# Kernel tuning notes

Measured on AMD Instinct MI355X. Metric: run time of the kernel, lower is better.

## Reference

```python
import jax, jax.numpy as jnp
import numpy as np

NL, D, NH, HD, MLP, L = 4, 1280, 16, 80, 5120, 2048
SEG = 512  # patches per packed image


def setup_inputs() -> dict:
    key = jax.random.key(0)
    ks = jax.random.split(key, 16)
    s = 0.02
    # per-segment RoPE frequency table: positions restart at each image boundary
    inv_freq = 1.0 / (10000.0 ** (jnp.arange(0, HD, 2, dtype=jnp.float32) / HD))  # (HD/2,)
    pos = (jnp.arange(L) % SEG).astype(jnp.float32)
    rotary_pos_emb = pos[:, None] * inv_freq[None, :]  # (L, HD/2)
    return {
        "x": jax.random.normal(ks[0], (L, D), jnp.float32),
        "rotary_pos_emb": rotary_pos_emb,
        "cu_seqlens": jnp.array([0, 512, 1024, 1536, 2048], jnp.int32),
        "ln1_g": 1.0 + s * jax.random.normal(ks[1], (NL, D), jnp.float32),
        "ln1_b": s * jax.random.normal(ks[2], (NL, D), jnp.float32),
        "ln2_g": 1.0 + s * jax.random.normal(ks[3], (NL, D), jnp.float32),
        "ln2_b": s * jax.random.normal(ks[4], (NL, D), jnp.float32),
        "qkv_w": s * jax.random.normal(ks[5], (NL, 3 * D, D), jnp.float32),
        "qkv_b": s * jax.random.normal(ks[6], (NL, 3 * D), jnp.float32),
        "proj_w": s * jax.random.normal(ks[7], (NL, D, D), jnp.float32),
        "proj_b": s * jax.random.normal(ks[8], (NL, D), jnp.float32),
        "mlp_w1": s * jax.random.normal(ks[9], (NL, MLP, D), jnp.float32),
        "mlp_b1": s * jax.random.normal(ks[10], (NL, MLP), jnp.float32),
        "mlp_w2": s * jax.random.normal(ks[11], (NL, D, MLP), jnp.float32),
        "mlp_b2": s * jax.random.normal(ks[12], (NL, D), jnp.float32),
    }


def _ln(x, g, b):
    m = jnp.mean(x, axis=-1, keepdims=True)
    v = jnp.mean((x - m) ** 2, axis=-1, keepdims=True)
    return (x - m) * jax.lax.rsqrt(v + 1e-6) * g + b


def _rope(t, cos, sin):
    # t: (L, H, HD); cos/sin: (L, 1, HD)
    half = t.shape[-1] // 2
    rot = jnp.concatenate([-t[..., half:], t[..., :half]], axis=-1)
    return t * cos + rot * sin


def reference(x, rotary_pos_emb, cu_seqlens, ln1_g, ln1_b, ln2_g, ln2_b,
              qkv_w, qkv_b, proj_w, proj_b, mlp_w1, mlp_b1, mlp_w2, mlp_b2):
    Lx = x.shape[0]
    cos = jnp.cos(rotary_pos_emb)
    sin = jnp.sin(rotary_pos_emb)
    cos = jnp.concatenate([cos, cos], axis=-1)[:, None, :]  # (L,1,HD)
    sin = jnp.concatenate([sin, sin], axis=-1)[:, None, :]
    # block-diagonal attention mask from cu_seqlens via segment ids
    seg = jnp.searchsorted(cu_seqlens, jnp.arange(Lx), side="right")  # (L,)
    mask = seg[:, None] == seg[None, :]  # (L,L) bool
    neg = jnp.finfo(jnp.float32).min
    scale = 1.0 / np.sqrt(HD)
    for l in range(qkv_w.shape[0]):
        h = _ln(x, ln1_g[l], ln1_b[l])
        qkv = (h @ qkv_w[l].T + qkv_b[l]).reshape(Lx, 3, NH, HD)
        q, k, v = qkv[:, 0], qkv[:, 1], qkv[:, 2]  # (L,H,HD) each
        q = _rope(q, cos, sin)
        k = _rope(k, cos, sin)
        scores = jnp.einsum("lhd,mhd->hlm", q, k) * scale  # (H,L,L)
        scores = jnp.where(mask[None], scores, neg)
        w = jax.nn.softmax(scores.astype(jnp.float32), axis=-1).astype(x.dtype)
        att = jnp.einsum("hlm,mhd->lhd", w, v).reshape(Lx, NH * HD)
        x = x + att @ proj_w[l].T + proj_b[l]
        h = _ln(x, ln2_g[l], ln2_b[l])
        x = x + jax.nn.gelu(h @ mlp_w1[l].T + mlp_b1[l], approximate=True) @ mlp_w2[l].T + mlp_b2[l]
    return x
```

## Files before the change

### kernel.cpp

```cpp
#include <hip/hip_runtime.h>
#include <cstdint>
#include <cstddef>

typedef unsigned short u16;
typedef __bf16 bf16_t;
typedef bf16_t bf16x8 __attribute__((ext_vector_type(8)));
typedef float f32x4 __attribute__((ext_vector_type(4)));

#define NLAY 4
#define DMODEL 1280
#define NHEAD 16
#define HDIM 80
#define HDP 96
#define MLPD 5120
#define LTOK 2048
#define SEGLEN 512

__device__ __forceinline__ u16 f2bf(float f) {
  union { float f; unsigned u; } x; x.f = f;
  unsigned r = x.u + 0x7fffu + ((x.u >> 16) & 1u);
  return (u16)(r >> 16);
}
__device__ __forceinline__ float bf2f(u16 s) {
  union { unsigned u; float f; } x; x.u = ((unsigned)s) << 16;
  return x.f;
}

#define GLOAD_LDS16(gsrc, ldst) \
  __builtin_amdgcn_global_load_lds((const __attribute__((address_space(1))) void*)(gsrc), \
                                   (__attribute__((address_space(3))) void*)(ldst), 16, 0, 0)

#define C0 (3 * DMODEL * DMODEL / 4)
#define C1 (C0 + DMODEL * DMODEL / 4)
#define C2 (C1 + MLPD * DMODEL / 4)
#define C3 (C2 + DMODEL * MLPD / 4)
__global__ __launch_bounds__(256) void cvt4(const float* __restrict__ s_q,
                                            const float* __restrict__ s_p,
                                            const float* __restrict__ s_1,
                                            const float* __restrict__ s_2,
                                            u16* __restrict__ o_q, u16* __restrict__ o_p,
                                            u16* __restrict__ o_1, u16* __restrict__ o_2) {
  int i = blockIdx.x * 256 + threadIdx.x;
  const float* src; u16* dst; int off;
  if (i < C0)      { src = s_q; dst = o_q; off = i; }
  else if (i < C1) { src = s_p; dst = o_p; off = i - C0; }
  else if (i < C2) { src = s_1; dst = o_1; off = i - C1; }
  else if (i < C3) { src = s_2; dst = o_2; off = i - C2; }
  else return;
  const float4 v = reinterpret_cast<const float4*>(src)[off];
  union { u16 s[4]; uint2 u; } o;
  o.s[0] = f2bf(v.x); o.s[1] = f2bf(v.y); o.s[2] = f2bf(v.z); o.s[3] = f2bf(v.w);
  reinterpret_cast<uint2*>(dst)[off] = o.u;
}

__global__ __launch_bounds__(256) void ln_bf16(const float* __restrict__ x,
                                               const float* __restrict__ g,
                                               const float* __restrict__ b,
                                               u16* __restrict__ out) {
  int row = blockIdx.x;
  int t = threadIdx.x;
  const float* xr = x + (size_t)row * DMODEL;
  float v[5]; float s = 0.f, s2 = 0.f;
#pragma unroll
  for (int i = 0; i < 5; i++) { v[i] = xr[t + i * 256]; s += v[i]; s2 += v[i] * v[i]; }
#pragma unroll
  for (int off = 32; off; off >>= 1) { s += __shfl_down(s, off); s2 += __shfl_down(s2, off); }
  __shared__ float ps[4], ps2[4];
  int w = t >> 6;
  if ((t & 63) == 0) { ps[w] = s; ps2[w] = s2; }
  __syncthreads();
  s = ps[0] + ps[1] + ps[2] + ps[3];
  s2 = ps2[0] + ps2[1] + ps2[2] + ps2[3];
  float mean = s * (1.f / DMODEL);
  float var = s2 * (1.f / DMODEL) - mean * mean;
  float inv = rsqrtf(var + 1e-6f);
#pragma unroll
  for (int i = 0; i < 5; i++) {
    int c = t + i * 256;
    out[(size_t)row * DMODEL + c] = f2bf((v[i] - mean) * inv * g[c] + b[c]);
  }
}

template <int EPI, int BM, int BN>
__global__ __launch_bounds__(256) void gemm_bt(const u16* __restrict__ A,
                                               const u16* __restrict__ B,
                                               const float* __restrict__ bias,
                                               float* __restrict__ Cf,
                                               u16* __restrict__ Cb,
                                               int M, int N, int K) {
  constexpr int MI = BM / 32;
  constexpr int NJ = BN / 32;
  constexpr int ACH = BM / 32;
  constexpr int BCH = BN / 32;
  __shared__ u16 As[2][BM * 64];
  __shared__ u16 Bs[2][BN * 64];

  int gN = gridDim.x, gM = gridDim.y;
  int flat = blockIdx.x + gN * blockIdx.y;
  int nwg = gN * gM;
  int qc = nwg >> 3, rc = nwg & 7;
  int xcd = flat & 7, pos = flat >> 3;
  int start = (xcd < rc) ? xcd * (qc + 1) : rc * (qc + 1) + (xcd - rc) * qc;
  int swz = start + pos;
  int m0 = (swz % gM) * BM;
  int n0 = (swz / gM) * BN;

  int t = threadIdx.x, lane = t & 63, w = t >> 6;
  int wm = w >> 1, wn = w & 1;
  int r = lane & 15, kq = lane >> 4;
  f32x4 acc[MI][NJ] = {};

  auto stage = [&](int buf, int k0) {
#pragma unroll
    for (int i = 0; i < ACH; i++) {
      int chunk = i * 256 + t;
      int row = chunk >> 3, s = chunk & 7;
      int ss = s ^ (row & 7);
      GLOAD_LDS16(A + (size_t)(m0 + row) * K + k0 + ss * 8, &As[buf][chunk * 8]);
    }
#pragma unroll
    for (int i = 0; i < BCH; i++) {
      int chunk = i * 256 + t;
      int row = chunk >> 3, s = chunk & 7;
      int ss = s ^ (row & 7);
      GLOAD_LDS16(B + (size_t)(n0 + row) * K + k0 + ss * 8, &Bs[buf][chunk * 8]);
    }
  };

  auto compute = [&](int buf) {
#pragma unroll
    for (int kk = 0; kk < 64; kk += 32) {
      int sx8 = (((kk >> 3) + kq) ^ (r & 7)) * 8;
      bf16x8 af[MI], bfr[NJ];
#pragma unroll
      for (int i = 0; i < MI; i++)
        af[i] = *(const bf16x8*)&As[buf][(wm * (BM / 2) + i * 16 + r) * 64 + sx8];
#pragma unroll
      for (int j = 0; j < NJ; j++)
        bfr[j] = *(const bf16x8*)&Bs[buf][(wn * (BN / 2) + j * 16 + r) * 64 + sx8];
#pragma unroll
      for (int i = 0; i < MI; i++)
#pragma unroll
        for (int j = 0; j < NJ; j++)
          acc[i][j] = __builtin_amdgcn_mfma_f32_16x16x32_bf16(af[i], bfr[j], acc[i][j], 0, 0, 0);
    }
  };

  int NT = K >> 6;
  stage(0, 0);
  __syncthreads();
  for (int step = 0; step < NT; step++) {
    int buf = step & 1;
    if (step + 1 < NT) stage(buf ^ 1, (step + 1) << 6);
    compute(buf);
    __syncthreads();
  }

#pragma unroll
  for (int i = 0; i < MI; i++) {
#pragma unroll
    for (int j = 0; j < NJ; j++) {
      int col = n0 + wn * (BN / 2) + j * 16 + r;
      float bv = bias[col];
#pragma unroll
      for (int reg = 0; reg < 4; reg++) {
        int rowg = m0 + wm * (BM / 2) + i * 16 + kq * 4 + reg;
        float val = acc[i][j][reg] + bv;
        if (EPI == 0) {
          Cf[(size_t)rowg * N + col] = val;
        } else if (EPI == 1) {
          Cf[(size_t)rowg * N + col] += val;
        } else if (EPI == 2) {
          float x3 = val * val * val;
          float gg = 0.5f * val * (1.f + tanhf(0.7978845608f * (val + 0.044715f * x3)));
          Cb[(size_t)rowg * N + col] = f2bf(gg);
        } else {
          Cb[(size_t)rowg * N + col] = f2bf(val);
        }
      }
    }
  }
}

__global__ __launch_bounds__(256) void rope_pack(const u16* __restrict__ qkv,
                                                 const float* __restrict__ rpe,
                                                 u16* __restrict__ qp,
                                                 u16* __restrict__ kp) {
  int l = blockIdx.x;
  int t = threadIdx.x;
  __shared__ float cs[40], sn[40];
  if (t < 40) {
    float a = rpe[l * 40 + t];
    cs[t] = cosf(a);
    sn[t] = sinf(a);
  }
  __syncthreads();
  const u16* row = qkv + (size_t)l * (3 * DMODEL);
  const float scale = 0.11180339887498949f;
#pragma unroll
  for (int i = 0; i < 5; i++) {
    int e = t + i * 256;
    int h = e / HDIM, d = e - h * HDIM;
    int dm = (d < 40) ? d : d - 40;
    float c = cs[dm], s = sn[dm];
    float qv = bf2f(row[h * HDIM + d]);
    float qr = (d < 40) ? -bf2f(row[h * HDIM + d + 40]) : bf2f(row[h * HDIM + d - 40]);
    qp[((size_t)h * LTOK + l) * HDP + d] = f2bf((qv * c + qr * s) * scale);
    float kv = bf2f(row[DMODEL + h * HDIM + d]);
    float kr = (d < 40) ? -bf2f(row[DMODEL + h * HDIM + d + 40]) : bf2f(row[DMODEL + h * HDIM + d - 40]);
    kp[((size_t)h * LTOK + l) * HDP + d] = f2bf(kv * c + kr * s);
  }
  {
    int h = t >> 4, p = t & 15;
    qp[((size_t)h * LTOK + l) * HDP + HDIM + p] = 0;
    kp[((size_t)h * LTOK + l) * HDP + HDIM + p] = 0;
  }
}

__global__ __launch_bounds__(256) void vtrans(const u16* __restrict__ qkv,
                                              u16* __restrict__ vt) {
  int blk = blockIdx.x;
  int h = blk >> 5, lt = blk & 31;
  int t = threadIdx.x;
  __shared__ u16 ld[64][81];
#pragma unroll
  for (int i = 0; i < 20; i++) {
    int idx = t + i * 256;
    int ll = idx / HDIM, d = idx - ll * HDIM;
    ld[ll][d] = qkv[(size_t)(lt * 64 + ll) * (3 * DMODEL) + 2 * DMODEL + h * HDIM + d];
  }
  __syncthreads();
#pragma unroll
  for (int i = 0; i < 20; i++) {
    int idx = t + i * 256;
    int d = idx >> 6, ll = idx & 63;
    vt[((size_t)h * HDIM + d) * LTOK + lt * 64 + ll] = ld[ll][d];
  }
}

__global__ __launch_bounds__(256) void attn(const u16* __restrict__ qp,
                                            const u16* __restrict__ kp,
                                            const u16* __restrict__ vt,
                                            u16* __restrict__ out) {
  int bid = blockIdx.x;
  int h = bid >> 5;
  int seg = (bid >> 3) & 3;
  int qt = bid & 7;
  int t = threadIdx.x, w = t >> 6, lane = t & 63;
  int r = lane & 15, kq = lane >> 4;
  __shared__ u16 P[4][16][512];
  int seg0 = seg * SEGLEN;
  int q0 = seg0 + qt * 64 + w * 16;

  bf16x8 qf[3];
  const u16* qrow = qp + ((size_t)h * LTOK + q0 + r) * HDP;
#pragma unroll
  for (int kk = 0; kk < 3; kk++) qf[kk] = *(const bf16x8*)(qrow + kk * 32 + kq * 8);

  f32x4 sc[32];
#pragma unroll
  for (int j = 0; j < 32; j++) {
    f32x4 a = {0.f, 0.f, 0.f, 0.f};
    const u16* krow = kp + ((size_t)h * LTOK + seg0 + j * 16 + r) * HDP;
#pragma unroll
    for (int kk = 0; kk < 3; kk++) {
      bf16x8 bfr = *(const bf16x8*)(krow + kk * 32 + kq * 8);
      a = __builtin_amdgcn_mfma_f32_16x16x32_bf16(qf[kk], bfr, a, 0, 0, 0);
    }
    sc[j] = a;
  }

#pragma unroll
  for (int rr = 0; rr < 4; rr++) {
    float m = -1e30f;
#pragma unroll
    for (int j = 0; j < 32; j++) m = fmaxf(m, sc[j][rr]);
#pragma unroll
    for (int off = 1; off < 16; off <<= 1) m = fmaxf(m, __shfl_xor(m, off));
    float s = 0.f;
#pragma unroll
    for (int j = 0; j < 32; j++) { float e = __expf(sc[j][rr] - m); sc[j][rr] = e; s += e; }
#pragma unroll
    for (int off = 1; off < 16; off <<= 1) s += __shfl_xor(s, off);
    float inv = 1.f / s;
#pragma unroll
    for (int j = 0; j < 32; j++)
      P[w][kq * 4 + rr][j * 16 + r] = f2bf(sc[j][rr] * inv);
  }
  __syncthreads();

  f32x4 oc[5] = {};
#pragma unroll
  for (int tt = 0; tt < 16; tt++) {
    bf16x8 a = *(const bf16x8*)&P[w][r][tt * 32 + kq * 8];
#pragma unroll
    for (int n = 0; n < 5; n++) {
      const u16* vrow = vt + ((size_t)h * HDIM + n * 16 + r) * LTOK + seg0 + tt * 32 + kq * 8;
      bf16x8 bfr = *(const bf16x8*)vrow;
      oc[n] = __builtin_amdgcn_mfma_f32_16x16x32_bf16(a, bfr, oc[n], 0, 0, 0);
    }
  }
#pragma unroll
  for (int n = 0; n < 5; n++)
#pragma unroll
    for (int reg = 0; reg < 4; reg++) {
      int l = q0 + kq * 4 + reg;
      out[(size_t)l * DMODEL + h * HDIM + n * 16 + r] = f2bf(oc[n][reg]);
    }
}

extern "C" void kernel_launch(void* const* d_in, const int* in_sizes, int n_in,
                              void* d_out, int out_size, void* d_ws, size_t ws_size,
                              hipStream_t stream) {
  (void)in_sizes; (void)n_in; (void)out_size; (void)ws_size;
  const float* x_in   = (const float*)d_in[0];
  const float* rpe    = (const float*)d_in[1];
  const float* ln1_g  = (const float*)d_in[3];
  const float* ln1_b  = (const float*)d_in[4];
  const float* ln2_g  = (const float*)d_in[5];
  const float* ln2_b  = (const float*)d_in[6];
  const float* qkv_w  = (const float*)d_in[7];
  const float* qkv_b  = (const float*)d_in[8];
  const float* proj_w = (const float*)d_in[9];
  const float* proj_b = (const float*)d_in[10];
  const float* mlp_w1 = (const float*)d_in[11];
  const float* mlp_b1 = (const float*)d_in[12];
  const float* mlp_w2 = (const float*)d_in[13];
  const float* mlp_b2 = (const float*)d_in[14];
  float* x = (float*)d_out;

  char* ws = (char*)d_ws;
  size_t off = 0;
  auto alloc = [&](size_t bytes) -> char* {
    char* p = ws + off;
    off = (off + bytes + 255) & ~(size_t)255;
    return p;
  };
  u16* wq  = (u16*)alloc((size_t)3 * DMODEL * DMODEL * 2);
  u16* wp  = (u16*)alloc((size_t)DMODEL * DMODEL * 2);
  u16* w1  = (u16*)alloc((size_t)MLPD * DMODEL * 2);
  u16* w2  = (u16*)alloc((size_t)DMODEL * MLPD * 2);
  u16* hb  = (u16*)alloc((size_t)LTOK * DMODEL * 2);
  u16* qkvb = (u16*)alloc((size_t)LTOK * 3 * DMODEL * 2);
  u16* qp  = (u16*)alloc((size_t)NHEAD * LTOK * HDP * 2);
  u16* kp  = (u16*)alloc((size_t)NHEAD * LTOK * HDP * 2);
  u16* vt  = (u16*)alloc((size_t)NHEAD * HDIM * LTOK * 2);
  u16* att = (u16*)alloc((size_t)LTOK * DMODEL * 2);
  u16* ge  = (u16*)alloc((size_t)LTOK * MLPD * 2);

  hipMemcpyAsync(x, x_in, (size_t)LTOK * DMODEL * sizeof(float),
                 hipMemcpyDeviceToDevice, stream);

  for (int l = 0; l < NLAY; l++) {
    cvt4<<<(C3 + 255) / 256, 256, 0, stream>>>(
        qkv_w + (size_t)l * 3 * DMODEL * DMODEL, proj_w + (size_t)l * DMODEL * DMODEL,
        mlp_w1 + (size_t)l * MLPD * DMODEL, mlp_w2 + (size_t)l * DMODEL * MLPD,
        wq, wp, w1, w2);

    ln_bf16<<<LTOK, 256, 0, stream>>>(x, ln1_g + l * DMODEL, ln1_b + l * DMODEL, hb);
    gemm_bt<3, 128, 128><<<dim3(30, 16), 256, 0, stream>>>(
        hb, wq, qkv_b + (size_t)l * 3 * DMODEL, nullptr, qkvb, LTOK, 3 * DMODEL, DMODEL);
    rope_pack<<<LTOK, 256, 0, stream>>>(qkvb, rpe, qp, kp);
    vtrans<<<NHEAD * 32, 256, 0, stream>>>(qkvb, vt);
    attn<<<NHEAD * 4 * 8, 256, 0, stream>>>(qp, kp, vt, att);
    gemm_bt<1, 64, 64><<<dim3(20, 32), 256, 0, stream>>>(
        att, wp, proj_b + (size_t)l * DMODEL, x, nullptr, LTOK, DMODEL, DMODEL);
    ln_bf16<<<LTOK, 256, 0, stream>>>(x, ln2_g + l * DMODEL, ln2_b + l * DMODEL, hb);
    gemm_bt<2, 128, 128><<<dim3(40, 16), 256, 0, stream>>>(
        hb, w1, mlp_b1 + (size_t)l * MLPD, nullptr, ge, LTOK, MLPD, DMODEL);
    gemm_bt<1, 64, 64><<<dim3(20, 32), 256, 0, stream>>>(
        ge, w2, mlp_b2 + (size_t)l * DMODEL, x, nullptr, LTOK, DMODEL, MLPD);
  }
}
```

Baseline: 1.008 ms.

## Add split-K with atomic accumulation, shrink GEMM tiles, use exp-based GELU

```diff
diff --git a/kernel.cpp b/kernel.cpp
--- a/kernel.cpp
+++ b/kernel.cpp
@@ -87,11 +87,11 @@
                                                const float* __restrict__ bias,
                                                float* __restrict__ Cf,
                                                u16* __restrict__ Cb,
-                                               int M, int N, int K) {
+                                               int M, int N, int K, int KC) {
   constexpr int MI = BM / 32;
   constexpr int NJ = BN / 32;
-  constexpr int ACH = BM / 32;
-  constexpr int BCH = BN / 32;
+  constexpr int ACH = BM * 64 / (256 * 8);
+  constexpr int BCH = BN * 64 / (256 * 8);
   __shared__ u16 As[2][BM * 64];
   __shared__ u16 Bs[2][BN * 64];
 
@@ -104,6 +104,7 @@
   int swz = start + pos;
   int m0 = (swz % gM) * BM;
   int n0 = (swz / gM) * BN;
+  int kbase = blockIdx.z * KC;
 
   int t = threadIdx.x, lane = t & 63, w = t >> 6;
   int wm = w >> 1, wn = w & 1;
@@ -146,12 +147,12 @@
     }
   };
 
-  int NT = K >> 6;
-  stage(0, 0);
+  int NT = KC >> 6;
+  stage(0, kbase);
   __syncthreads();
   for (int step = 0; step < NT; step++) {
     int buf = step & 1;
-    if (step + 1 < NT) stage(buf ^ 1, (step + 1) << 6);
+    if (step + 1 < NT) stage(buf ^ 1, kbase + (step + 1) * 64);
     compute(buf);
     __syncthreads();
   }
@@ -161,7 +162,7 @@
 #pragma unroll
     for (int j = 0; j < NJ; j++) {
       int col = n0 + wn * (BN / 2) + j * 16 + r;
-      float bv = bias[col];
+      float bv = (EPI == 4 && blockIdx.z != 0) ? 0.f : bias[col];
 #pragma unroll
       for (int reg = 0; reg < 4; reg++) {
         int rowg = m0 + wm * (BM / 2) + i * 16 + kq * 4 + reg;
@@ -171,11 +172,13 @@
         } else if (EPI == 1) {
           Cf[(size_t)rowg * N + col] += val;
         } else if (EPI == 2) {
-          float x3 = val * val * val;
-          float gg = 0.5f * val * (1.f + tanhf(0.7978845608f * (val + 0.044715f * x3)));
+          float z2 = -1.5957691216057308f * fmaf(0.044715f * val, val * val, val);
+          float gg = val / (1.f + __expf(z2));
           Cb[(size_t)rowg * N + col] = f2bf(gg);
+        } else if (EPI == 3) {
+          Cb[(size_t)rowg * N + col] = f2bf(val);
         } else {
-          Cb[(size_t)rowg * N + col] = f2bf(val);
+          atomicAdd(&Cf[(size_t)rowg * N + col], val);
         }
       }
     }
@@ -358,17 +361,21 @@
         wq, wp, w1, w2);
 
     ln_bf16<<<LTOK, 256, 0, stream>>>(x, ln1_g + l * DMODEL, ln1_b + l * DMODEL, hb);
-    gemm_bt<3, 128, 128><<<dim3(30, 16), 256, 0, stream>>>(
-        hb, wq, qkv_b + (size_t)l * 3 * DMODEL, nullptr, qkvb, LTOK, 3 * DMODEL, DMODEL);
+    gemm_bt<3, 64, 64><<<dim3(60, 32, 1), 256, 0, stream>>>(
+        hb, wq, qkv_b + (size_t)l * 3 * DMODEL, nullptr, qkvb,
+        LTOK, 3 * DMODEL, DMODEL, DMODEL);
     rope_pack<<<LTOK, 256, 0, stream>>>(qkvb, rpe, qp, kp);
     vtrans<<<NHEAD * 32, 256, 0, stream>>>(qkvb, vt);
     attn<<<NHEAD * 4 * 8, 256, 0, stream>>>(qp, kp, vt, att);
-    gemm_bt<1, 64, 64><<<dim3(20, 32), 256, 0, stream>>>(
-        att, wp, proj_b + (size_t)l * DMODEL, x, nullptr, LTOK, DMODEL, DMODEL);
+    gemm_bt<4, 64, 64><<<dim3(20, 32, 2), 256, 0, stream>>>(
+        att, wp, proj_b + (size_t)l * DMODEL, x, nullptr,
+        LTOK, DMODEL, DMODEL, DMODEL / 2);
     ln_bf16<<<LTOK, 256, 0, stream>>>(x, ln2_g + l * DMODEL, ln2_b + l * DMODEL, hb);
-    gemm_bt<2, 128, 128><<<dim3(40, 16), 256, 0, stream>>>(
-        hb, w1, mlp_b1 + (size_t)l * MLPD, nullptr, ge, LTOK, MLPD, DMODEL);
-    gemm_bt<1, 64, 64><<<dim3(20, 32), 256, 0, stream>>>(
-        ge, w2, mlp_b2 + (size_t)l * DMODEL, x, nullptr, LTOK, DMODEL, MLPD);
-  }
-}
+    gemm_bt<2, 64, 64><<<dim3(80, 32, 1), 256, 0, stream>>>(
+        hb, w1, mlp_b1 + (size_t)l * MLPD, nullptr, ge,
+        LTOK, MLPD, DMODEL, DMODEL);
+    gemm_bt<4, 64, 64><<<dim3(20, 32, 4), 256, 0, stream>>>(
+        ge, w2, mlp_b2 + (size_t)l * DMODEL, x, nullptr,
+        LTOK, DMODEL, MLPD, MLPD / 4);
+  }
+}
```

After: 1.081 ms. 1.07x slower.

## Add 256x128 triple-buffered 8-wave GEMM for QKV and MLP-up projections

Applied to the files above, without the earlier changes.

```diff
diff --git a/kernel.cpp b/kernel.cpp
--- a/kernel.cpp
+++ b/kernel.cpp
@@ -29,6 +29,10 @@
 #define GLOAD_LDS16(gsrc, ldst) \
   __builtin_amdgcn_global_load_lds((const __attribute__((address_space(1))) void*)(gsrc), \
                                    (__attribute__((address_space(3))) void*)(ldst), 16, 0, 0)
+
+__device__ __forceinline__ void barrier_mem() {
+  asm volatile("s_barrier" ::: "memory");
+}
 
 #define C0 (3 * DMODEL * DMODEL / 4)
 #define C1 (C0 + DMODEL * DMODEL / 4)
@@ -81,6 +85,136 @@
   }
 }
 
+template <int EPI>
+__global__ __launch_bounds__(512) void gemm8(const u16* __restrict__ A,
+                                             const u16* __restrict__ B,
+                                             const float* __restrict__ bias,
+                                             u16* __restrict__ Cb,
+                                             int M, int N, int K) {
+  __shared__ u16 As[3][256 * 64];
+  __shared__ u16 Bs[3][128 * 64];
+
+  int gN = gridDim.x, gM = gridDim.y;
+  int flat = blockIdx.x + gN * blockIdx.y;
+  int nwg = gN * gM;
+  int qc = nwg >> 3, rc = nwg & 7;
+  int xcd = flat & 7, pos = flat >> 3;
+  int start = (xcd < rc) ? xcd * (qc + 1) : rc * (qc + 1) + (xcd - rc) * qc;
+  int swz = start + pos;
+  int m0 = (swz % gM) * 256;
+  int n0 = (swz / gM) * 128;
+
+  int t = threadIdx.x, lane = t & 63, w = t >> 6;
+  int wm = w >> 1, wn = w & 1;
+  int r = lane & 15, kq = lane >> 4;
+  f32x4 acc[4][4] = {};
+
+  auto stageA = [&](int buf, int k0, int half) {
+#pragma unroll
+    for (int i = 0; i < 2; i++) {
+      int chunk = half * 1024 + i * 512 + t;
+      int row = chunk >> 3, s = chunk & 7;
+      int ss = s ^ (row & 7);
+      GLOAD_LDS16(A + (size_t)(m0 + row) * K + k0 + ss * 8, &As[buf][chunk * 8]);
+    }
+  };
+  auto stageB = [&](int buf, int k0) {
+#pragma unroll
+    for (int i = 0; i < 2; i++) {
+      int chunk = i * 512 + t;
+      int row = chunk >> 3, s = chunk & 7;
+      int ss = s ^ (row & 7);
+      GLOAD_LDS16(B + (size_t)(n0 + row) * K + k0 + ss * 8, &Bs[buf][chunk * 8]);
+    }
+  };
+
+  bf16x8 af[2][2], bf[2][2];
+  auto loadA = [&](const u16* as, int mh) {
+#pragma unroll
+    for (int i2 = 0; i2 < 2; i2++)
+#pragma unroll
+      for (int ks = 0; ks < 2; ks++) {
+        int row = wm * 64 + (2 * mh + i2) * 16 + r;
+        int sx8 = (ks * 4 + kq) ^ (r & 7);
+        af[i2][ks] = *(const bf16x8*)&as[row * 64 + sx8 * 8];
+      }
+  };
+  auto loadB = [&](const u16* bs, int nh) {
+#pragma unroll
+    for (int j2 = 0; j2 < 2; j2++)
+#pragma unroll
+      for (int ks = 0; ks < 2; ks++) {
+        int row = wn * 64 + (2 * nh + j2) * 16 + r;
+        int sx8 = (ks * 4 + kq) ^ (r & 7);
+        bf[j2][ks] = *(const bf16x8*)&bs[row * 64 + sx8 * 8];
+      }
+  };
+  auto mfma8 = [&](int mh, int nh) {
+    __builtin_amdgcn_s_setprio(1);
+#pragma unroll
+    for (int i2 = 0; i2 < 2; i2++)
+#pragma unroll
+      for (int j2 = 0; j2 < 2; j2++)
+#pragma unroll
+        for (int ks = 0; ks < 2; ks++)
+          acc[2 * mh + i2][2 * nh + j2] = __builtin_amdgcn_mfma_f32_16x16x32_bf16(
+              af[i2][ks], bf[j2][ks], acc[2 * mh + i2][2 * nh + j2], 0, 0, 0);
+    __builtin_amdgcn_s_setprio(0);
+  };
+
+  int NT = K >> 6;
+  stageA(0, 0, 0); stageA(0, 0, 1); stageB(0, 0);
+  stageA(1, 64, 0); stageA(1, 64, 1); stageB(1, 64);
+
+  int bt = 0;
+  for (int kt = 0; kt < NT; kt++) {
+    if (kt == NT - 1) asm volatile("s_waitcnt vmcnt(0)" ::: "memory");
+    else              asm volatile("s_waitcnt vmcnt(6)" ::: "memory");
+    barrier_mem();
+    const u16* as = As[bt];
+    const u16* bs = Bs[bt];
+    int b2 = bt + 2; if (b2 >= 3) b2 -= 3;
+    int k2 = (kt + 2) << 6;
+    bool st = (kt + 2) < NT;
+    loadA(as, 0); loadB(bs, 0);
+    if (st) stageA(b2, k2, 0);
+    mfma8(0, 0);
+    barrier_mem();
+    loadB(bs, 1);
+    if (st) stageA(b2, k2, 1);
+    mfma8(0, 1);
+    barrier_mem();
+    loadA(as, 1);
+    if (st) stageB(b2, k2);
+    mfma8(1, 1);
+    barrier_mem();
+    loadB(bs, 0);
+    mfma8(1, 0);
+    bt++; if (bt == 3) bt = 0;
+  }
+
+#pragma unroll
+  for (int i = 0; i < 4; i++) {
+#pragma unroll
+    for (int j = 0; j < 4; j++) {
+      int col = n0 + wn * 64 + j * 16 + r;
+      float bv = bias[col];
+#pragma unroll
+      for (int reg = 0; reg < 4; reg++) {
+        int rowg = m0 + wm * 64 + i * 16 + kq * 4 + reg;
+        float val = acc[i][j][reg] + bv;
+        if (EPI == 2) {
+          float z2 = -1.5957691216057308f * fmaf(0.044715f * val, val * val, val);
+          float gg = val / (1.f + __expf(z2));
+          Cb[(size_t)rowg * N + col] = f2bf(gg);
+        } else {
+          Cb[(size_t)rowg * N + col] = f2bf(val);
+        }
+      }
+    }
+  }
+}
+
 template <int EPI, int BM, int BN>
 __global__ __launch_bounds__(256) void gemm_bt(const u16* __restrict__ A,
                                                const u16* __restrict__ B,
@@ -90,8 +224,8 @@
                                                int M, int N, int K) {
   constexpr int MI = BM / 32;
   constexpr int NJ = BN / 32;
-  constexpr int ACH = BM / 32;
-  constexpr int BCH = BN / 32;
+  constexpr int ACH = BM * 64 / (256 * 8);
+  constexpr int BCH = BN * 64 / (256 * 8);
   __shared__ u16 As[2][BM * 64];
   __shared__ u16 Bs[2][BN * 64];
 
@@ -151,7 +285,7 @@
   __syncthreads();
   for (int step = 0; step < NT; step++) {
     int buf = step & 1;
-    if (step + 1 < NT) stage(buf ^ 1, (step + 1) << 6);
+    if (step + 1 < NT) stage(buf ^ 1, (step + 1) * 64);
     compute(buf);
     __syncthreads();
   }
@@ -166,14 +300,8 @@
       for (int reg = 0; reg < 4; reg++) {
         int rowg = m0 + wm * (BM / 2) + i * 16 + kq * 4 + reg;
         float val = acc[i][j][reg] + bv;
-        if (EPI == 0) {
-          Cf[(size_t)rowg * N + col] = val;
-        } else if (EPI == 1) {
+        if (EPI == 1) {
           Cf[(size_t)rowg * N + col] += val;
-        } else if (EPI == 2) {
-          float x3 = val * val * val;
-          float gg = 0.5f * val * (1.f + tanhf(0.7978845608f * (val + 0.044715f * x3)));
-          Cb[(size_t)rowg * N + col] = f2bf(gg);
         } else {
           Cb[(size_t)rowg * N + col] = f2bf(val);
         }
@@ -358,16 +486,16 @@
         wq, wp, w1, w2);
 
     ln_bf16<<<LTOK, 256, 0, stream>>>(x, ln1_g + l * DMODEL, ln1_b + l * DMODEL, hb);
-    gemm_bt<3, 128, 128><<<dim3(30, 16), 256, 0, stream>>>(
-        hb, wq, qkv_b + (size_t)l * 3 * DMODEL, nullptr, qkvb, LTOK, 3 * DMODEL, DMODEL);
+    gemm8<3><<<dim3(30, 8), 512, 0, stream>>>(
+        hb, wq, qkv_b + (size_t)l * 3 * DMODEL, qkvb, LTOK, 3 * DMODEL, DMODEL);
     rope_pack<<<LTOK, 256, 0, stream>>>(qkvb, rpe, qp, kp);
     vtrans<<<NHEAD * 32, 256, 0, stream>>>(qkvb, vt);
     attn<<<NHEAD * 4 * 8, 256, 0, stream>>>(qp, kp, vt, att);
     gemm_bt<1, 64, 64><<<dim3(20, 32), 256, 0, stream>>>(
         att, wp, proj_b + (size_t)l * DMODEL, x, nullptr, LTOK, DMODEL, DMODEL);
     ln_bf16<<<LTOK, 256, 0, stream>>>(x, ln2_g + l * DMODEL, ln2_b + l * DMODEL, hb);
-    gemm_bt<2, 128, 128><<<dim3(40, 16), 256, 0, stream>>>(
-        hb, w1, mlp_b1 + (size_t)l * MLPD, nullptr, ge, LTOK, MLPD, DMODEL);
+    gemm8<2><<<dim3(40, 8), 512, 0, stream>>>(
+        hb, w1, mlp_b1 + (size_t)l * MLPD, ge, LTOK, MLPD, DMODEL);
     gemm_bt<1, 64, 64><<<dim3(20, 32), 256, 0, stream>>>(
         ge, w2, mlp_b2 + (size_t)l * DMODEL, x, nullptr, LTOK, DMODEL, MLPD);
   }
```

Measured after the change: 1.019 ms. Within noise of the previous version (+1.1%).
